# Kernel tuning notes

Measured on AMD Instinct MI355X. Metric: run time of the kernel, lower is better.

Reference implementation:

```python
import jax, jax.numpy as jnp
import numpy as np

H = 16   # n_heads == n_I
D = 64   # d_q = d_k = d_v = d_r
DX = H * D
B, S = 4, 2048

def setup_inputs() -> dict:
    key = jax.random.key(0)
    ks = jax.random.split(key, 9)
    sc = 0.02
    return {
        "value": jax.random.normal(ks[0], (B, S, DX), jnp.float32),
        "key":   jax.random.normal(ks[1], (B, S, DX), jnp.float32),
        "query": jax.random.normal(ks[2], (B, S, DX), jnp.float32),
        "Wq_w": jax.random.normal(ks[3], (DX, DX), jnp.float32) * sc,
        "Wq_b": jnp.zeros((DX,), jnp.float32),
        "Wk_w": jax.random.normal(ks[4], (DX, DX), jnp.float32) * sc,
        "Wk_b": jnp.zeros((DX,), jnp.float32),
        "Wv_w": jax.random.normal(ks[5], (DX, DX), jnp.float32) * sc,
        "Wv_b": jnp.zeros((DX,), jnp.float32),
        "Wr_w": jax.random.normal(ks[6], (DX, DX), jnp.float32) * sc,
        "Wr_b": jnp.zeros((DX,), jnp.float32),
        "Wout_w": jax.random.normal(ks[7], (DX, DX), jnp.float32) * sc,
        "Wout_b": jnp.zeros((DX,), jnp.float32),
    }

def _heads(x, b, s):
    # [b, s, H*D] -> [b, H, s, D]
    return x.reshape(b, s, H, D).transpose(0, 2, 1, 3)

def reference(value, key, query, Wq_w, Wq_b, Wk_w, Wk_b, Wv_w, Wv_b,
              Wr_w, Wr_b, Wout_w, Wout_b):
    b, s, _ = query.shape
    # torch nn.Linear: y = x @ W.T + b
    Q = _heads(query @ Wq_w.T + Wq_b, b, s)   # [b,H,s,D]
    K = _heads(key   @ Wk_w.T + Wk_b, b, s)
    V = _heads(value @ Wv_w.T + Wv_b, b, s)
    R = _heads(query @ Wr_w.T + Wr_b, b, s)
    dot_scale = jnp.sqrt(jnp.float32(D))
    scores = jnp.einsum("bhid,bhjd->bhij", Q, K) / dot_scale  # [b,H,s,s]
    attn = jax.nn.softmax(scores, axis=-1)                    # dropout p=0
    out = jnp.einsum("bhij,bhjd->bhid", attn, V)              # [b,H,s,D]
    out = out * R                                             # R-gating
    out = out.transpose(0, 2, 1, 3).reshape(b, s, H * D)
    return out @ Wout_w.T + Wout_b
```

## Files before the change

kernel.cpp:

```cpp
#include <hip/hip_runtime.h>
#include <hip/hip_bf16.h>

typedef __bf16 bf16;
typedef __bf16 bf16x4 __attribute__((ext_vector_type(4)));
typedef __bf16 bf16x8 __attribute__((ext_vector_type(8)));
typedef float  f32x4  __attribute__((ext_vector_type(4)));

#define MFMA_16x16x32(a, b, c) __builtin_amdgcn_mfma_f32_16x16x32_bf16((a), (b), (c), 0, 0, 0)

typedef const void __attribute__((address_space(1))) gvoid;
typedef void __attribute__((address_space(3))) svoid;

__device__ __forceinline__ void async_copy16(const void* gptr, void* ldsptr) {
    __builtin_amdgcn_global_load_lds((gvoid*)gptr, (svoid*)ldsptr, 16, 0, 0);
}

__device__ __forceinline__ int swz8(int row, int quad) {
    return (quad ^ ((row >> 1) & 3)) * 8;
}

__global__ void cvt3_acts(const float* __restrict__ s0, const float* __restrict__ s1,
                          const float* __restrict__ s2,
                          bf16* __restrict__ d0, bf16* __restrict__ d1, bf16* __restrict__ d2)
{
    constexpr int N4SEG = 8192 * 1024 / 4;
    int i = blockIdx.x * blockDim.x + threadIdx.x;
    const int stride = gridDim.x * blockDim.x;
    for (; i < 3 * N4SEG; i += stride) {
        const int seg = i / N4SEG;
        const int j = i - seg * N4SEG;
        const float* s = seg == 0 ? s0 : (seg == 1 ? s1 : s2);
        bf16* d = seg == 0 ? d0 : (seg == 1 ? d1 : d2);
        float4 v = ((const float4*)s)[j];
        bf16x4 o = { (bf16)v.x, (bf16)v.y, (bf16)v.z, (bf16)v.w };
        ((bf16x4*)d)[j] = o;
    }
}

__global__ void cvt5_wts(const float* __restrict__ s0, const float* __restrict__ s1,
                         const float* __restrict__ s2, const float* __restrict__ s3,
                         const float* __restrict__ s4,
                         bf16* __restrict__ d0, bf16* __restrict__ d1, bf16* __restrict__ d2,
                         bf16* __restrict__ d3, bf16* __restrict__ d4)
{
    constexpr int N4SEG = 1024 * 1024 / 4;
    int i = blockIdx.x * blockDim.x + threadIdx.x;
    const int stride = gridDim.x * blockDim.x;
    for (; i < 5 * N4SEG; i += stride) {
        const int seg = i / N4SEG;
        const int j = i - seg * N4SEG;
        const float* s = seg == 0 ? s0 : seg == 1 ? s1 : seg == 2 ? s2 : seg == 3 ? s3 : s4;
        bf16* d = seg == 0 ? d0 : seg == 1 ? d1 : seg == 2 ? d2 : seg == 3 ? d3 : d4;
        float4 v = ((const float4*)s)[j];
        bf16x4 o = { (bf16)v.x, (bf16)v.y, (bf16)v.z, (bf16)v.w };
        ((bf16x4*)d)[j] = o;
    }
}

__global__ void proj_fused(const bf16* __restrict__ xq, const bf16* __restrict__ xk,
                           const bf16* __restrict__ xv, const bf16* __restrict__ wall,
                           const float* __restrict__ ball,
                           bf16* __restrict__ qr, bf16* __restrict__ kws,
                           bf16* __restrict__ vtws)
{
    constexpr int K = 1024, SDIM = 2048;
    __shared__ alignas(16) bf16 As[2][128 * 32];
    __shared__ alignas(16) bf16 Bs[2][128 * 32];

    const int tid  = threadIdx.x;
    const int lane = tid & 63;
    const int wave = tid >> 6;
    const int wm   = wave >> 1;
    const int wn   = wave & 1;
    const int bm   = blockIdx.x * 128;
    const int by   = blockIdx.y;
    const int bn   = by * 128;
    const int l15  = lane & 15;
    const int quad = lane >> 4;

    const bf16* X = (by < 16) ? xq : (by < 24 ? xk : xv);

    const int srow = lane >> 2;
    const int scol = (lane & 3) * 8;

    const bf16* aseg0 = X + (size_t)(bm + wave * 32 + srow) * K + scol;
    const bf16* aseg1 = X + (size_t)(bm + wave * 32 + 16 + srow) * K + scol;
    const bf16* bseg0 = wall + (size_t)(bn + wave * 32 + srow) * K + scol;
    const bf16* bseg1 = wall + (size_t)(bn + wave * 32 + 16 + srow) * K + scol;

    f32x4 acc[4][4] = {};

    async_copy16(aseg0, As[0] + (wave * 2 + 0) * 512);
    async_copy16(aseg1, As[0] + (wave * 2 + 1) * 512);
    async_copy16(bseg0, Bs[0] + (wave * 2 + 0) * 512);
    async_copy16(bseg1, Bs[0] + (wave * 2 + 1) * 512);

    for (int k0 = 0; k0 < K; k0 += 32) {
        const int cur = (k0 >> 5) & 1;
        __syncthreads();
        if (k0 + 32 < K) {
            const int nxt = cur ^ 1;
            async_copy16(aseg0 + k0 + 32, As[nxt] + (wave * 2 + 0) * 512);
            async_copy16(aseg1 + k0 + 32, As[nxt] + (wave * 2 + 1) * 512);
            async_copy16(bseg0 + k0 + 32, Bs[nxt] + (wave * 2 + 0) * 512);
            async_copy16(bseg1 + k0 + 32, Bs[nxt] + (wave * 2 + 1) * 512);
        }

        bf16x8 af[4], bfr[4];
        #pragma unroll
        for (int i = 0; i < 4; ++i)
            af[i] = *(const bf16x8*)(As[cur] + (wm * 64 + i * 16 + l15) * 32 + quad * 8);
        #pragma unroll
        for (int j = 0; j < 4; ++j)
            bfr[j] = *(const bf16x8*)(Bs[cur] + (wn * 64 + j * 16 + l15) * 32 + quad * 8);
        #pragma unroll
        for (int i = 0; i < 4; ++i)
            #pragma unroll
            for (int j = 0; j < 4; ++j)
                acc[i][j] = MFMA_16x16x32(af[i], bfr[j], acc[i][j]);
    }

    #pragma unroll
    for (int i = 0; i < 4; ++i) {
        const int rowg = bm + wm * 64 + i * 16 + quad * 4;
        #pragma unroll
        for (int j = 0; j < 4; ++j) {
            const int colg = bn + wn * 64 + j * 16 + l15;
            const float bv = ball[colg];
            if (by < 16) {
                #pragma unroll
                for (int r = 0; r < 4; ++r)
                    qr[(size_t)(rowg + r) * 2048 + colg] = (bf16)(acc[i][j][r] + bv);
            } else if (by < 24) {
                const int cl = colg - 2048;
                #pragma unroll
                for (int r = 0; r < 4; ++r)
                    kws[(size_t)(rowg + r) * 1024 + cl] = (bf16)(acc[i][j][r] + bv);
            } else {
                const int d = colg - 3072;
                bf16x4 o;
                #pragma unroll
                for (int r = 0; r < 4; ++r) o[r] = (bf16)(acc[i][j][r] + bv);
                *(bf16x4*)(vtws + (size_t)(rowg >> 11) * 1024 * SDIM
                                + (size_t)d * SDIM + (rowg & (SDIM - 1))) = o;
            }
        }
    }
}

__global__ void gemm_out(const bf16* __restrict__ X, const bf16* __restrict__ W,
                         const float* __restrict__ bias, float* __restrict__ Y)
{
    constexpr int K = 1024, N = 1024;
    __shared__ alignas(16) bf16 As[2][128 * 32];
    __shared__ alignas(16) bf16 Bs[2][128 * 32];

    const int tid  = threadIdx.x;
    const int lane = tid & 63;
    const int wave = tid >> 6;
    const int wm   = wave >> 1;
    const int wn   = wave & 1;
    const int bm   = blockIdx.x * 128;
    const int bn   = blockIdx.y * 128;
    const int l15  = lane & 15;
    const int quad = lane >> 4;

    const int srow = lane >> 2;
    const int scol = (lane & 3) * 8;

    const bf16* aseg0 = X + (size_t)(bm + wave * 32 + srow) * K + scol;
    const bf16* aseg1 = X + (size_t)(bm + wave * 32 + 16 + srow) * K + scol;
    const bf16* bseg0 = W + (size_t)(bn + wave * 32 + srow) * K + scol;
    const bf16* bseg1 = W + (size_t)(bn + wave * 32 + 16 + srow) * K + scol;

    f32x4 acc[4][4] = {};

    async_copy16(aseg0, As[0] + (wave * 2 + 0) * 512);
    async_copy16(aseg1, As[0] + (wave * 2 + 1) * 512);
    async_copy16(bseg0, Bs[0] + (wave * 2 + 0) * 512);
    async_copy16(bseg1, Bs[0] + (wave * 2 + 1) * 512);

    for (int k0 = 0; k0 < K; k0 += 32) {
        const int cur = (k0 >> 5) & 1;
        __syncthreads();
        if (k0 + 32 < K) {
            const int nxt = cur ^ 1;
            async_copy16(aseg0 + k0 + 32, As[nxt] + (wave * 2 + 0) * 512);
            async_copy16(aseg1 + k0 + 32, As[nxt] + (wave * 2 + 1) * 512);
            async_copy16(bseg0 + k0 + 32, Bs[nxt] + (wave * 2 + 0) * 512);
            async_copy16(bseg1 + k0 + 32, Bs[nxt] + (wave * 2 + 1) * 512);
        }

        bf16x8 af[4], bfr[4];
        #pragma unroll
        for (int i = 0; i < 4; ++i)
            af[i] = *(const bf16x8*)(As[cur] + (wm * 64 + i * 16 + l15) * 32 + quad * 8);
        #pragma unroll
        for (int j = 0; j < 4; ++j)
            bfr[j] = *(const bf16x8*)(Bs[cur] + (wn * 64 + j * 16 + l15) * 32 + quad * 8);
        #pragma unroll
        for (int i = 0; i < 4; ++i)
            #pragma unroll
            for (int j = 0; j < 4; ++j)
                acc[i][j] = MFMA_16x16x32(af[i], bfr[j], acc[i][j]);
    }

    #pragma unroll
    for (int i = 0; i < 4; ++i) {
        const int rowg = bm + wm * 64 + i * 16 + quad * 4;
        #pragma unroll
        for (int j = 0; j < 4; ++j) {
            const int colg = bn + wn * 64 + j * 16 + l15;
            const float bv = bias[colg];
            #pragma unroll
            for (int r = 0; r < 4; ++r)
                Y[(size_t)(rowg + r) * N + colg] = acc[i][j][r] + bv;
        }
    }
}

__launch_bounds__(256, 4)
__global__ void attn_fused(const bf16* __restrict__ QRp, const bf16* __restrict__ Kp,
                           const bf16* __restrict__ Vtp, bf16* __restrict__ Op)
{
    constexpr int S = 2048, DXc = 1024, QRST = 2048, Dh = 64;
    constexpr int PST = 40;
    __shared__ alignas(16) bf16 Ks[2][64 * 32];
    __shared__ alignas(16) bf16 Vt[2][64 * 32];
    __shared__ alignas(16) bf16 Pt[4][2][16 * PST];

    const int tid  = threadIdx.x;
    const int lane = tid & 63;
    const int wave = tid >> 6;
    const int qt = blockIdx.x, h = blockIdx.y, b = blockIdx.z;
    const int l15  = lane & 15;
    const int quad = lane >> 4;

    const size_t qrbase = ((size_t)b * S) * QRST + h * Dh;
    const size_t kbase  = ((size_t)b * S) * DXc + h * Dh;
    const size_t vtbase = ((size_t)(b * 16 + h) * Dh) * S;
    const size_t obase  = ((size_t)b * S) * DXc + h * Dh;

    constexpr float QSCALE = 0.125f * 1.44269504088896340736f;
    bf16x8 qf[2][2];
    #pragma unroll
    for (int mi = 0; mi < 2; ++mi) {
        const int qrow = qt * 128 + wave * 32 + mi * 16 + l15;
        const bf16* qptr = QRp + qrbase + (size_t)qrow * QRST + quad * 8;
        qf[mi][0] = *(const bf16x8*)(qptr);
        qf[mi][1] = *(const bf16x8*)(qptr + 32);
        #pragma unroll
        for (int j = 0; j < 8; ++j) {
            qf[mi][0][j] = (bf16)((float)qf[mi][0][j] * QSCALE);
            qf[mi][1][j] = (bf16)((float)qf[mi][1][j] * QSCALE);
        }
    }

    bf16x8 onef;
    #pragma unroll
    for (int j = 0; j < 8; ++j) onef[j] = (bf16)1.0f;

    f32x4 oacc[2][4] = {};
    f32x4 lsacc[2] = {};

    const int srow = lane >> 2;
    const int scol = ((lane & 3) ^ ((srow >> 1) & 3)) * 8;
    const bf16* kseg = Kp  + kbase  + (size_t)(16 * wave + srow) * DXc + scol;
    const bf16* vseg = Vtp + vtbase + (size_t)(16 * wave + srow) * S   + scol;
    const int soff = wave * 512;

    for (int kv0 = 0; kv0 < S; kv0 += 64) {
        __syncthreads();
        async_copy16(kseg + (size_t)kv0 * DXc,      &Ks[0][soff]);
        async_copy16(kseg + (size_t)kv0 * DXc + 32, &Ks[1][soff]);
        async_copy16(vseg + kv0,                    &Vt[0][soff]);
        async_copy16(vseg + kv0 + 32,               &Vt[1][soff]);
        __syncthreads();

        #pragma unroll
        for (int half = 0; half < 2; ++half) {
            f32x4 st[2][2];
            #pragma unroll
            for (int nbl = 0; nbl < 2; ++nbl) {
                const int nb = half * 2 + nbl;
                bf16x8 kf0 = *(const bf16x8*)(&Ks[0][0] + (nb * 16 + l15) * 32 + swz8(l15, quad));
                bf16x8 kf1 = *(const bf16x8*)(&Ks[1][0] + (nb * 16 + l15) * 32 + swz8(l15, quad));
                #pragma unroll
                for (int mi = 0; mi < 2; ++mi) {
                    f32x4 z = {0.f, 0.f, 0.f, 0.f};
                    z = MFMA_16x16x32(kf1, qf[mi][1], z);
                    st[mi][nbl] = MFMA_16x16x32(kf0, qf[mi][0], z);
                }
            }
            #pragma unroll
            for (int mi = 0; mi < 2; ++mi) {
                #pragma unroll
                for (int nbl = 0; nbl < 2; ++nbl) {
                    bf16x4 pt;
                    #pragma unroll
                    for (int r = 0; r < 4; ++r)
                        pt[r] = (bf16)__builtin_exp2f(st[mi][nbl][r]);
                    *(bf16x4*)(&Pt[wave][mi][0] + l15 * PST
                               + nbl * 16 + quad * 4) = pt;
                }
            }
            const bf16* vb = &Vt[half][0];
            bf16x8 vtf[4];
            #pragma unroll
            for (int db = 0; db < 4; ++db)
                vtf[db] = *(const bf16x8*)(vb + (db * 16 + l15) * 32 + swz8(l15, quad));
            #pragma unroll
            for (int mi = 0; mi < 2; ++mi) {
                bf16x8 pf = *(const bf16x8*)(&Pt[wave][mi][0] + l15 * PST + quad * 8);
                #pragma unroll
                for (int db = 0; db < 4; ++db)
                    oacc[mi][db] = MFMA_16x16x32(vtf[db], pf, oacc[mi][db]);
                lsacc[mi] = MFMA_16x16x32(onef, pf, lsacc[mi]);
            }
        }
    }

    #pragma unroll
    for (int mi = 0; mi < 2; ++mi) {
        const float inv = 1.0f / lsacc[mi][0];
        const int qrow = qt * 128 + wave * 32 + mi * 16 + l15;
        const bf16* rrow = QRp + qrbase + (size_t)qrow * QRST + 1024;
        bf16* orow = Op + obase + (size_t)qrow * DXc;
        #pragma unroll
        for (int db = 0; db < 4; ++db) {
            bf16x4 rg = *(const bf16x4*)(rrow + db * 16 + quad * 4);
            bf16x4 o;
            #pragma unroll
            for (int r = 0; r < 4; ++r)
                o[r] = (bf16)(oacc[mi][db][r] * inv * (float)rg[r]);
            *(bf16x4*)(orow + db * 16 + quad * 4) = o;
        }
    }
}

extern "C" void kernel_launch(void* const* d_in, const int* in_sizes, int n_in,
                              void* d_out, int out_size, void* d_ws, size_t ws_size,
                              hipStream_t stream)
{
    (void)in_sizes; (void)n_in; (void)out_size; (void)ws_size;
    constexpr int B = 4, S = 2048, DX = 1024, M = B * S;
    constexpr size_t MD = (size_t)M * DX;
    constexpr size_t WD = (size_t)DX * DX;

    const float* value  = (const float*)d_in[0];
    const float* keyi   = (const float*)d_in[1];
    const float* query  = (const float*)d_in[2];
    const float* Wq_w   = (const float*)d_in[3];
    const float* Wq_b   = (const float*)d_in[4];
    const float* Wk_w   = (const float*)d_in[5];
    const float* Wk_b   = (const float*)d_in[6];
    const float* Wv_w   = (const float*)d_in[7];
    const float* Wv_b   = (const float*)d_in[8];
    const float* Wr_w   = (const float*)d_in[9];
    const float* Wr_b   = (const float*)d_in[10];
    const float* Wout_w = (const float*)d_in[11];
    const float* Wout_b = (const float*)d_in[12];

    bf16* p = (bf16*)d_ws;
    bf16* xv   = p;  p += MD;
    bf16* xk   = p;  p += MD;
    bf16* xq   = p;  p += MD;
    bf16* wall = p;  p += 4 * WD;
    bf16* wo   = p;  p += WD;
    bf16* qr   = p;  p += 2 * MD;
    bf16* kws  = p;  p += MD;
    bf16* vtws = p;  p += MD;
    float* ball = (float*)p;
    bf16* ows = xv;

    hipMemcpyAsync(ball,            Wq_b, DX * sizeof(float), hipMemcpyDeviceToDevice, stream);
    hipMemcpyAsync(ball + DX,       Wr_b, DX * sizeof(float), hipMemcpyDeviceToDevice, stream);
    hipMemcpyAsync(ball + 2 * DX,   Wk_b, DX * sizeof(float), hipMemcpyDeviceToDevice, stream);
    hipMemcpyAsync(ball + 3 * DX,   Wv_b, DX * sizeof(float), hipMemcpyDeviceToDevice, stream);

    cvt3_acts<<<dim3(2048), dim3(256), 0, stream>>>(value, keyi, query, xv, xk, xq);
    cvt5_wts <<<dim3(1024), dim3(256), 0, stream>>>(Wq_w, Wr_w, Wk_w, Wv_w, Wout_w,
                                                    wall, wall + WD, wall + 2 * WD,
                                                    wall + 3 * WD, wo);

    proj_fused<<<dim3(M / 128, 32), dim3(256), 0, stream>>>(
        xq, xk, xv, wall, ball, qr, kws, vtws);

    attn_fused<<<dim3(S / 128, 16, B), dim3(256), 0, stream>>>(qr, kws, vtws, ows);

    gemm_out<<<dim3(M / 128, DX / 128), dim3(256), 0, stream>>>(
        ows, wo, Wout_b, (float*)d_out);
}
```

Measured before the change: 399.4 us.

## Double-buffer K/V tiles in attention to overlap loads with MFMA compute

Splits the K and V LDS tiles into two buffers. The next 64-key tile is prefetched with async global-to-LDS copies while the current tile is being computed, which cuts the barriers per iteration from two to one. The P staging buffer is cut to a single slice per wave, with the write and read of P interleaved per query sub-block, and the V fragment loads are moved before the softmax exponentials. This hides global load latency behind compute but raises LDS use per block, which could limit occupancy.

```diff
diff --git a/kernel.cpp b/kernel.cpp
--- a/kernel.cpp
+++ b/kernel.cpp
@@ -225,9 +225,10 @@
 {
     constexpr int S = 2048, DXc = 1024, QRST = 2048, Dh = 64;
     constexpr int PST = 40;
-    __shared__ alignas(16) bf16 Ks[2][64 * 32];
-    __shared__ alignas(16) bf16 Vt[2][64 * 32];
-    __shared__ alignas(16) bf16 Pt[4][2][16 * PST];
+    constexpr int NT = S / 64;
+    __shared__ alignas(16) bf16 Ks[2][2][64 * 32];
+    __shared__ alignas(16) bf16 Vt[2][2][64 * 32];
+    __shared__ alignas(16) bf16 Pt[4][16 * PST];
 
     const int tid  = threadIdx.x;
     const int lane = tid & 63;
@@ -240,6 +241,17 @@
     const size_t kbase  = ((size_t)b * S) * DXc + h * Dh;
     const size_t vtbase = ((size_t)(b * 16 + h) * Dh) * S;
     const size_t obase  = ((size_t)b * S) * DXc + h * Dh;
+
+    const int srow = lane >> 2;
+    const int scol = ((lane & 3) ^ ((srow >> 1) & 3)) * 8;
+    const bf16* kseg = Kp  + kbase  + (size_t)(16 * wave + srow) * DXc + scol;
+    const bf16* vseg = Vtp + vtbase + (size_t)(16 * wave + srow) * S   + scol;
+    const int soff = wave * 512;
+
+    async_copy16(kseg,      &Ks[0][0][soff]);
+    async_copy16(kseg + 32, &Ks[0][1][soff]);
+    async_copy16(vseg,      &Vt[0][0][soff]);
+    async_copy16(vseg + 32, &Vt[0][1][soff]);
 
     constexpr float QSCALE = 0.125f * 1.44269504088896340736f;
     bf16x8 qf[2][2];
@@ -263,19 +275,18 @@
     f32x4 oacc[2][4] = {};
     f32x4 lsacc[2] = {};
 
-    const int srow = lane >> 2;
-    const int scol = ((lane & 3) ^ ((srow >> 1) & 3)) * 8;
-    const bf16* kseg = Kp  + kbase  + (size_t)(16 * wave + srow) * DXc + scol;
-    const bf16* vseg = Vtp + vtbase + (size_t)(16 * wave + srow) * S   + scol;
-    const int soff = wave * 512;
-
-    for (int kv0 = 0; kv0 < S; kv0 += 64) {
+    for (int t = 0; t < NT; ++t) {
+        const int cur = t & 1;
         __syncthreads();
-        async_copy16(kseg + (size_t)kv0 * DXc,      &Ks[0][soff]);
-        async_copy16(kseg + (size_t)kv0 * DXc + 32, &Ks[1][soff]);
-        async_copy16(vseg + kv0,                    &Vt[0][soff]);
-        async_copy16(vseg + kv0 + 32,               &Vt[1][soff]);
-        __syncthreads();
+        if (t + 1 < NT) {
+            const int nxt = cur ^ 1;
+            const size_t ko = (size_t)(t + 1) * 64 * DXc;
+            const int    vo = (t + 1) * 64;
+            async_copy16(kseg + ko,      &Ks[nxt][0][soff]);
+            async_copy16(kseg + ko + 32, &Ks[nxt][1][soff]);
+            async_copy16(vseg + vo,      &Vt[nxt][0][soff]);
+            async_copy16(vseg + vo + 32, &Vt[nxt][1][soff]);
+        }
 
         #pragma unroll
         for (int half = 0; half < 2; ++half) {
@@ -283,8 +294,8 @@
             #pragma unroll
             for (int nbl = 0; nbl < 2; ++nbl) {
                 const int nb = half * 2 + nbl;
-                bf16x8 kf0 = *(const bf16x8*)(&Ks[0][0] + (nb * 16 + l15) * 32 + swz8(l15, quad));
-                bf16x8 kf1 = *(const bf16x8*)(&Ks[1][0] + (nb * 16 + l15) * 32 + swz8(l15, quad));
+                bf16x8 kf0 = *(const bf16x8*)(&Ks[cur][0][0] + (nb * 16 + l15) * 32 + swz8(l15, quad));
+                bf16x8 kf1 = *(const bf16x8*)(&Ks[cur][1][0] + (nb * 16 + l15) * 32 + swz8(l15, quad));
                 #pragma unroll
                 for (int mi = 0; mi < 2; ++mi) {
                     f32x4 z = {0.f, 0.f, 0.f, 0.f};
@@ -292,6 +303,11 @@
                     st[mi][nbl] = MFMA_16x16x32(kf0, qf[mi][0], z);
                 }
             }
+            const bf16* vb = &Vt[cur][half][0];
+            bf16x8 vtf[4];
+            #pragma unroll
+            for (int db = 0; db < 4; ++db)
+                vtf[db] = *(const bf16x8*)(vb + (db * 16 + l15) * 32 + swz8(l15, quad));
             #pragma unroll
             for (int mi = 0; mi < 2; ++mi) {
                 #pragma unroll
@@ -300,18 +316,9 @@
                     #pragma unroll
                     for (int r = 0; r < 4; ++r)
                         pt[r] = (bf16)__builtin_exp2f(st[mi][nbl][r]);
-                    *(bf16x4*)(&Pt[wave][mi][0] + l15 * PST
-                               + nbl * 16 + quad * 4) = pt;
+                    *(bf16x4*)(&Pt[wave][0] + l15 * PST + nbl * 16 + quad * 4) = pt;
                 }
-            }
-            const bf16* vb = &Vt[half][0];
-            bf16x8 vtf[4];
-            #pragma unroll
-            for (int db = 0; db < 4; ++db)
-                vtf[db] = *(const bf16x8*)(vb + (db * 16 + l15) * 32 + swz8(l15, quad));
-            #pragma unroll
-            for (int mi = 0; mi < 2; ++mi) {
-                bf16x8 pf = *(const bf16x8*)(&Pt[wave][mi][0] + l15 * PST + quad * 8);
+                bf16x8 pf = *(const bf16x8*)(&Pt[wave][0] + l15 * PST + quad * 8);
                 #pragma unroll
                 for (int db = 0; db < 4; ++db)
                     oacc[mi][db] = MFMA_16x16x32(vtf[db], pf, oacc[mi][db]);
```

Result: no change. 399.6 us (+0.1%).
